# Kernel tuning notes

Hardware: AMD Instinct MI355X
Metric: run time of the kernel (lower is better)

Reference implementation:

```python
import jax, jax.numpy as jnp
import numpy as np

N_NODES = 50000
N_EDGES = 500000
D = 128
R = 8
L = 2
BN_EPS = 1e-5


def setup_inputs() -> dict:
    key = jax.random.key(0)
    ks = jax.random.split(key, 8)
    x = jax.random.normal(ks[0], (N_NODES, D), dtype=jnp.float32)
    xe = jax.random.normal(ks[1], (N_EDGES, D), dtype=jnp.float32)
    edge_index = jax.random.randint(ks[2], (2, N_EDGES), 0, N_NODES, dtype=jnp.int64)
    edge_type = jax.random.randint(ks[3], (N_EDGES,), 0, R, dtype=jnp.int64)
    # glorot init for weight/root, zeros bias; BN affine params
    w_scale = jnp.sqrt(6.0 / (D + D))
    weight = jax.random.uniform(ks[4], (L, R, D, D), jnp.float32, -w_scale, w_scale)
    root = jax.random.uniform(ks[5], (L, D, D), jnp.float32, -w_scale, w_scale)
    bias = jnp.zeros((L, D), jnp.float32)
    bn_gamma = jnp.ones((L, D), jnp.float32)
    bn_beta = jnp.zeros((L, D), jnp.float32)
    return {"x": x, "xe": xe, "edge_index": edge_index, "edge_type": edge_type,
            "weight": weight, "root": root, "bias": bias,
            "bn_gamma": bn_gamma, "bn_beta": bn_beta}


def _rgcn_edge_conv(h, xe, src, dst, etype, w, rt, b):
    # message: relu(x_j + xe) per edge (independent of relation mask)
    m = jax.nn.relu(h[src] + xe)                         # [E, D]
    # mean-aggregate per (relation, dst) via a combined segment id
    n = h.shape[0]
    seg = etype * n + dst                                # [E]
    sums = jax.ops.segment_sum(m, seg, num_segments=R * n)            # [R*N, D]
    cnt = jax.ops.segment_sum(jnp.ones((m.shape[0],), m.dtype), seg,
                              num_segments=R * n)                     # [R*N]
    mean = sums / jnp.maximum(cnt, 1.0)[:, None]
    hr = mean.reshape(R, n, -1)                          # [R, N, D]
    out = jnp.einsum('rnd,rdo->no', hr, w)               # sum_i H_i @ W_i
    out = out + h @ rt + b
    return out


def _batch_norm(h, gamma, beta):
    mu = h.mean(axis=0)
    var = jnp.mean((h - mu) ** 2, axis=0)  # biased, as torch BN (training)
    return (h - mu) * jax.lax.rsqrt(var + BN_EPS) * gamma + beta


def reference(x, xe, edge_index, edge_type, weight, root, bias, bn_gamma, bn_beta):
    src, dst = edge_index[0], edge_index[1]
    h = x
    for l in range(L):
        h = _rgcn_edge_conv(h, xe, src, dst, edge_type, weight[l], root[l], bias[l])
        h = _batch_norm(h, bn_gamma[l], bn_beta[l])
        if l != L - 1:
            h = jax.nn.relu(h)
        # drop_ratio=0 -> dropout is identity
    return h  # JK='last'
```

## Files before the change

### kernel.cpp

```cpp
#include <hip/hip_runtime.h>
#include <hip/hip_bf16.h>

typedef __attribute__((ext_vector_type(8))) short bf16x8;
typedef __attribute__((ext_vector_type(4))) float f32x4;

constexpr int D = 128;
constexpr int R = 8;
constexpr float BN_EPS = 1e-5f;

__device__ __forceinline__ unsigned short f2bf(float x) {
  __hip_bfloat16 b = __float2bfloat16(x);
  union { __hip_bfloat16 b; unsigned short u; } c; c.b = b; return c.u;
}

__global__ __launch_bounds__(256) void hist_k(const int* __restrict__ ei,
                                              const int* __restrict__ et,
                                              int* __restrict__ cnt, int E) {
  int e = blockIdx.x * 256 + threadIdx.x;
  if (e >= E) return;
  atomicAdd(&cnt[ei[E + e] * 8 + et[e]], 1);
}

__global__ __launch_bounds__(256) void scan_partial_k(const int* __restrict__ cnt,
                                                      int* __restrict__ offs,
                                                      int* __restrict__ bsum, int NK) {
  __shared__ int s[256];
  int tid = threadIdx.x;
  int base = blockIdx.x * 4096 + tid * 16;
  int loc[16];
  int sum = 0;
  #pragma unroll
  for (int i = 0; i < 16; ++i) {
    int idx = base + i;
    int v = (idx < NK) ? cnt[idx] : 0;
    loc[i] = sum; sum += v;
  }
  s[tid] = sum;
  __syncthreads();
  if (tid == 0) {
    int run = 0;
    for (int i = 0; i < 256; ++i) { int t = s[i]; s[i] = run; run += t; }
    bsum[blockIdx.x] = run;
  }
  __syncthreads();
  int off = s[tid];
  #pragma unroll
  for (int i = 0; i < 16; ++i) {
    int idx = base + i;
    if (idx < NK) offs[idx] = off + loc[i];
  }
}

__global__ void scan_bsums_k(int* __restrict__ bsum, int nb) {
  if (threadIdx.x == 0 && blockIdx.x == 0) {
    int run = 0;
    for (int b = 0; b < nb; ++b) { int t = bsum[b]; bsum[b] = run; run += t; }
  }
}

__global__ __launch_bounds__(256) void scan_addback_k(int* __restrict__ offs,
                                                      const int* __restrict__ bsum,
                                                      int NK, int E) {
  int idx = blockIdx.x * 256 + threadIdx.x;
  if (idx < NK) offs[idx] += bsum[idx >> 12];
  if (idx == 0) offs[NK] = E;
}

__global__ __launch_bounds__(256) void place_k(const int* __restrict__ ei,
                                               const int* __restrict__ et,
                                               const int* __restrict__ offs,
                                               int* __restrict__ cnt,
                                               int2* __restrict__ pairs, int E) {
  int e = blockIdx.x * 256 + threadIdx.x;
  if (e >= E) return;
  int key = ei[E + e] * 8 + et[e];
  int pos = offs[key] + atomicAdd(&cnt[key], 1);
  pairs[pos] = make_int2(e, ei[e]);
}

__device__ __forceinline__ void edge_acc(float4& acc, int e, int s, int c,
                                         const float* __restrict__ h,
                                         const float* __restrict__ xe) {
  float4 xv = ((const float4*)xe)[(size_t)e * 32 + c];
  float4 hv = ((const float4*)h)[(size_t)s * 32 + c];
  acc.x += fmaxf(xv.x + hv.x, 0.f);
  acc.y += fmaxf(xv.y + hv.y, 0.f);
  acc.z += fmaxf(xv.z + hv.z, 0.f);
  acc.w += fmaxf(xv.w + hv.w, 0.f);
}

__global__ __launch_bounds__(256) void agg_k(const float* __restrict__ h,
                                             const float* __restrict__ xe,
                                             const int2* __restrict__ pairs,
                                             const int* __restrict__ offs,
                                             unsigned short* __restrict__ Mb, int NK) {
  int grp = threadIdx.x >> 5;
  int s0 = (blockIdx.x * 8 + grp) * 4;
  if (s0 >= NK) return;
  int c = threadIdx.x & 31;

  int4 ov = *(const int4*)(offs + s0);
  int o4 = offs[s0 + 4];
  int st[4] = {ov.x, ov.y, ov.z, ov.w};
  int en[4] = {ov.y, ov.z, ov.w, o4};

  int2 pr[4];
  #pragma unroll
  for (int j = 0; j < 4; ++j) {
    int m = en[j] - st[j];
    if (m > 0) pr[j] = pairs[st[j] + min(c, min(m, 32) - 1)];
  }

  float4 acc[4];
  #pragma unroll
  for (int j = 0; j < 4; ++j) acc[j] = make_float4(0.f, 0.f, 0.f, 0.f);

  #pragma unroll
  for (int j = 0; j < 4; ++j) {
    int m = en[j] - st[j];
    if (m > 0) {
      int mm = min(m, 32);
      {
        int e0 = __shfl(pr[j].x, 0, 32), sB = __shfl(pr[j].y, 0, 32);
        edge_acc(acc[j], e0, sB, c, h, xe);
      }
      if (mm >= 2) { edge_acc(acc[j], __shfl(pr[j].x, 1, 32), __shfl(pr[j].y, 1, 32), c, h, xe); }
      if (mm >= 3) { edge_acc(acc[j], __shfl(pr[j].x, 2, 32), __shfl(pr[j].y, 2, 32), c, h, xe); }
      if (mm >= 4) { edge_acc(acc[j], __shfl(pr[j].x, 3, 32), __shfl(pr[j].y, 3, 32), c, h, xe); }
      for (int i = 4; i < mm; ++i)
        edge_acc(acc[j], __shfl(pr[j].x, i, 32), __shfl(pr[j].y, i, 32), c, h, xe);
      for (int base = st[j] + 32; base < en[j]; base += 32) {
        int mm2 = min(32, en[j] - base);
        int2 pr2 = pairs[base + min(c, mm2 - 1)];
        for (int i = 0; i < mm2; ++i)
          edge_acc(acc[j], __shfl(pr2.x, i, 32), __shfl(pr2.y, i, 32), c, h, xe);
      }
    }
  }

  int pos = (c >> 3) * 32 + (c & 3) * 8 + ((c >> 2) & 1) * 4;
  #pragma unroll
  for (int j = 0; j < 4; ++j) {
    int len = en[j] - st[j];
    float inv = (len > 0) ? 1.0f / (float)len : 0.f;
    ushort4 u;
    u.x = f2bf(acc[j].x * inv); u.y = f2bf(acc[j].y * inv);
    u.z = f2bf(acc[j].z * inv); u.w = f2bf(acc[j].w * inv);
    *(ushort4*)(Mb + (size_t)(s0 + j) * 128 + pos) = u;
  }
}

__global__ __launch_bounds__(256) void cast_swz_k(const float* __restrict__ in,
                                                  unsigned short* __restrict__ outb, int n4) {
  int gi = blockIdx.x * 256 + threadIdx.x;
  if (gi >= n4) return;
  int n = gi >> 5, c = gi & 31;
  float4 v = ((const float4*)in)[gi];
  int pos = (c >> 3) * 32 + (c & 3) * 8 + ((c >> 2) & 1) * 4;
  ushort4 u;
  u.x = f2bf(v.x); u.y = f2bf(v.y); u.z = f2bf(v.z); u.w = f2bf(v.w);
  *(ushort4*)(outb + (size_t)n * 128 + pos) = u;
}

__global__ __launch_bounds__(256) void wcast_k(const float* __restrict__ W,
                                               const float* __restrict__ root,
                                               unsigned short* __restrict__ Whi) {
  int idx = blockIdx.x * 256 + threadIdx.x;
  if (idx >= 1152 * 128) return;
  int k = idx >> 7, col = idx & 127;
  float w = (k < 1024) ? W[idx] : root[idx - 1024 * 128];
  int kk = k & 31;
  int pos = (k & ~31) + ((kk & 15) >> 2) * 8 + (kk >> 4) * 4 + (kk & 3);
  Whi[col * 1152 + pos] = f2bf(w);
}

__global__ __launch_bounds__(256) void gemm_k(
    const unsigned short* __restrict__ Mb,
    const unsigned short* __restrict__ hb,
    const unsigned short* __restrict__ Whi,
    const float* __restrict__ bias,
    float* __restrict__ out,
    float* __restrict__ colstats, int N) {
  __shared__ float ldsS[128], ldsQ[128];
  const int tid = threadIdx.x;
  const int wv = tid >> 6, lane = tid & 63;
  const int lr = lane & 15, g = lane >> 4;
  const int r0 = blockIdx.x * 128;
  const int cf0 = wv * 2;

  int row[8];
  #pragma unroll
  for (int rf = 0; rf < 8; ++rf) row[rf] = min(r0 + rf * 16 + lr, N - 1);

  const unsigned short* pb0 = Whi + (size_t)(cf0 * 16 + lr) * 1152 + g * 8;
  const unsigned short* pb1 = pb0 + 16 * 1152;

  f32x4 acc[8][2];
  #pragma unroll
  for (int a = 0; a < 8; ++a)
    #pragma unroll
    for (int b = 0; b < 2; ++b) acc[a][b] = (f32x4){0.f, 0.f, 0.f, 0.f};

  #pragma unroll 2
  for (int t = 0; t < 32; ++t) {
    bf16x8 b0 = *(const bf16x8*)(pb0 + t * 32);
    bf16x8 b1 = *(const bf16x8*)(pb1 + t * 32);
    #pragma unroll
    for (int rf = 0; rf < 8; ++rf) {
      bf16x8 a = *(const bf16x8*)(Mb + (size_t)row[rf] * 1024 + t * 32 + g * 8);
      acc[rf][0] = __builtin_amdgcn_mfma_f32_16x16x32_bf16(a, b0, acc[rf][0], 0, 0, 0);
      acc[rf][1] = __builtin_amdgcn_mfma_f32_16x16x32_bf16(a, b1, acc[rf][1], 0, 0, 0);
    }
  }
  #pragma unroll
  for (int tt = 0; tt < 4; ++tt) {
    bf16x8 b0 = *(const bf16x8*)(pb0 + 1024 + tt * 32);
    bf16x8 b1 = *(const bf16x8*)(pb1 + 1024 + tt * 32);
    #pragma unroll
    for (int rf = 0; rf < 8; ++rf) {
      bf16x8 a = *(const bf16x8*)(hb + (size_t)row[rf] * 128 + tt * 32 + g * 8);
      acc[rf][0] = __builtin_amdgcn_mfma_f32_16x16x32_bf16(a, b0, acc[rf][0], 0, 0, 0);
      acc[rf][1] = __builtin_amdgcn_mfma_f32_16x16x32_bf16(a, b1, acc[rf][1], 0, 0, 0);
    }
  }

  #pragma unroll
  for (int c = 0; c < 2; ++c) {
    int col = (cf0 + c) * 16 + lr;
    float bs = bias[col];
    float s = 0.f, q = 0.f;
    #pragma unroll
    for (int rf = 0; rf < 8; ++rf) {
      #pragma unroll
      for (int j = 0; j < 4; ++j) {
        int r = r0 + rf * 16 + g * 4 + j;
        if (r < N) {
          float v = acc[rf][c][j] + bs;
          out[(size_t)r * 128 + col] = v;
          s += v; q += v * v;
        }
      }
    }
    s += __shfl_xor(s, 16); s += __shfl_xor(s, 32);
    q += __shfl_xor(q, 16); q += __shfl_xor(q, 32);
    if (g == 0) { ldsS[col] = s; ldsQ[col] = q; }
  }
  __syncthreads();
  if (tid < 128) {
    atomicAdd(&colstats[tid], ldsS[tid]);
    atomicAdd(&colstats[128 + tid], ldsQ[tid]);
  }
}

__global__ __launch_bounds__(256) void bn_apply_k(
    const float* __restrict__ in, float* __restrict__ out,
    unsigned short* __restrict__ hbOut,
    const float* __restrict__ colstats,
    const float* __restrict__ gamma, const float* __restrict__ beta,
    int N, int doRelu) {
  int gi = blockIdx.x * 256 + threadIdx.x;
  if (gi >= N * 32) return;
  int n = gi >> 5, c = gi & 31;
  int c0 = c * 4;
  float invN = 1.0f / (float)N;
  float4 v = ((const float4*)in)[gi];
  float4 o;
  #pragma unroll
  for (int j = 0; j < 4; ++j) {
    int cc = c0 + j;
    float mu = colstats[cc] * invN;
    float var = colstats[128 + cc] * invN - mu * mu;
    float scale = rsqrtf(var + BN_EPS) * gamma[cc];
    float shift = beta[cc] - mu * scale;
    float x = (j == 0) ? v.x : (j == 1) ? v.y : (j == 2) ? v.z : v.w;
    float y = x * scale + shift;
    if (doRelu) y = fmaxf(y, 0.f);
    if (j == 0) o.x = y; else if (j == 1) o.y = y; else if (j == 2) o.z = y; else o.w = y;
  }
  ((float4*)out)[gi] = o;
  if (hbOut) {
    int pos = (c >> 3) * 32 + (c & 3) * 8 + ((c >> 2) & 1) * 4;
    ushort4 u;
    u.x = f2bf(o.x); u.y = f2bf(o.y); u.z = f2bf(o.z); u.w = f2bf(o.w);
    *(ushort4*)(hbOut + (size_t)n * 128 + pos) = u;
  }
}

extern "C" void kernel_launch(void* const* d_in, const int* in_sizes, int n_in,
                              void* d_out, int out_size, void* d_ws, size_t ws_size,
                              hipStream_t stream) {
  const float* x      = (const float*)d_in[0];
  const float* xe     = (const float*)d_in[1];
  const int*   ei     = (const int*)d_in[2];
  const int*   et     = (const int*)d_in[3];
  const float* weight = (const float*)d_in[4];
  const float* root   = (const float*)d_in[5];
  const float* bias   = (const float*)d_in[6];
  const float* gamma  = (const float*)d_in[7];
  const float* beta   = (const float*)d_in[8];
  float* out = (float*)d_out;

  const int N = in_sizes[0] / D;
  const int E = in_sizes[3];
  const int NK = N * R;

  char* w = (char*)d_ws;
  size_t off = 0;
  auto alloc = [&](size_t bytes) { char* p = w + off; off = (off + bytes + 255) & ~(size_t)255; return p; };
  unsigned short* Mb   = (unsigned short*)alloc((size_t)NK * 128 * 2);
  unsigned short* hb   = (unsigned short*)alloc((size_t)N * 128 * 2);
  float*          h1   = (float*)alloc((size_t)N * 128 * 4);
  unsigned short* Whi  = (unsigned short*)alloc(1152 * 128 * 2);
  int*            offs = (int*)alloc((size_t)(NK + 1) * 4);
  int*            cnt  = (int*)alloc((size_t)NK * 4);
  int2*           pairs= (int2*)alloc((size_t)E * 8);
  int*            bsum = (int*)alloc(512 * 4);
  float*          cst  = (float*)alloc(256 * 4);

  const int NB = (NK + 4095) / 4096;

  hipMemsetAsync(cnt, 0, (size_t)NK * 4, stream);
  hist_k<<<(E + 255) / 256, 256, 0, stream>>>(ei, et, cnt, E);
  scan_partial_k<<<NB, 256, 0, stream>>>(cnt, offs, bsum, NK);
  scan_bsums_k<<<1, 64, 0, stream>>>(bsum, NB);
  scan_addback_k<<<(NK + 255) / 256, 256, 0, stream>>>(offs, bsum, NK, E);
  hipMemsetAsync(cnt, 0, (size_t)NK * 4, stream);
  place_k<<<(E + 255) / 256, 256, 0, stream>>>(ei, et, offs, cnt, pairs, E);

  const int aggBlocks  = (NK + 31) / 32;
  const int gemmBlocks = (N + 127) / 128;
  const int castBlocks = (N * 32 + 255) / 256;

  for (int l = 0; l < 2; ++l) {
    const float* hin = (l == 0) ? x : h1;
    float* opre      = (l == 0) ? h1 : out;

    wcast_k<<<576, 256, 0, stream>>>(weight + (size_t)l * 1024 * 128,
                                     root + (size_t)l * 128 * 128, Whi);
    agg_k<<<aggBlocks, 256, 0, stream>>>(hin, xe, pairs, offs, Mb, NK);
    if (l == 0)
      cast_swz_k<<<castBlocks, 256, 0, stream>>>(x, hb, N * 32);
    hipMemsetAsync(cst, 0, 256 * 4, stream);
    gemm_k<<<gemmBlocks, 256, 0, stream>>>(Mb, hb, Whi,
                                           bias + (size_t)l * D, opre, cst, N);
    bn_apply_k<<<castBlocks, 256, 0, stream>>>(
        opre, opre, (l == 0) ? hb : (unsigned short*)nullptr,
        cst, gamma + (size_t)l * D, beta + (size_t)l * D, N, (l == 0) ? 1 : 0);
  }
}
```

Baseline: 484.3 us.

## Cache edge features as bf16 in edge-sorted order and prefetch GEMM A tiles

In layer 0 the aggregation kernel writes each edge's features, converted to bf16, into a buffer ordered by sorted edge position. Layer 1 then reads this compact buffer sequentially instead of gathering fp32 xe rows at random, which halves the bytes and makes the reads contiguous. The GEMM merges its relation and root loops into one loop and register-prefetches the next A fragments to hide load latency. The cost is an extra 128MB write in layer 0, bf16 rounding of xe in layer 1, and higher register pressure in the GEMM.

```diff
diff --git a/kernel.cpp b/kernel.cpp
--- a/kernel.cpp
+++ b/kernel.cpp
@@ -11,6 +11,9 @@
 __device__ __forceinline__ unsigned short f2bf(float x) {
   __hip_bfloat16 b = __float2bfloat16(x);
   union { __hip_bfloat16 b; unsigned short u; } c; c.b = b; return c.u;
+}
+__device__ __forceinline__ float bf2f(unsigned short u) {
+  union { float f; unsigned int i; } c; c.i = ((unsigned int)u) << 16; return c.f;
 }
 
 __global__ __launch_bounds__(256) void hist_k(const int* __restrict__ ei,
@@ -78,10 +81,21 @@
   pairs[pos] = make_int2(e, ei[e]);
 }
 
-__device__ __forceinline__ void edge_acc(float4& acc, int e, int s, int c,
-                                         const float* __restrict__ h,
-                                         const float* __restrict__ xe) {
-  float4 xv = ((const float4*)xe)[(size_t)e * 32 + c];
+template <int XMODE>
+__device__ __forceinline__ void edge_proc(float4& acc, int pos, int e, int s, int c,
+                                          const float* __restrict__ h,
+                                          const float* __restrict__ xe,
+                                          unsigned short* __restrict__ xep) {
+  float4 xv;
+  if (XMODE == 0) {
+    xv = ((const float4*)xe)[(size_t)e * 32 + c];
+    ushort4 u;
+    u.x = f2bf(xv.x); u.y = f2bf(xv.y); u.z = f2bf(xv.z); u.w = f2bf(xv.w);
+    *(ushort4*)(xep + (size_t)pos * 128 + c * 4) = u;
+  } else {
+    ushort4 u = *(const ushort4*)(xep + (size_t)pos * 128 + c * 4);
+    xv.x = bf2f(u.x); xv.y = bf2f(u.y); xv.z = bf2f(u.z); xv.w = bf2f(u.w);
+  }
   float4 hv = ((const float4*)h)[(size_t)s * 32 + c];
   acc.x += fmaxf(xv.x + hv.x, 0.f);
   acc.y += fmaxf(xv.y + hv.y, 0.f);
@@ -89,8 +103,10 @@
   acc.w += fmaxf(xv.w + hv.w, 0.f);
 }
 
+template <int XMODE>
 __global__ __launch_bounds__(256) void agg_k(const float* __restrict__ h,
                                              const float* __restrict__ xe,
+                                             unsigned short* __restrict__ xep,
                                              const int2* __restrict__ pairs,
                                              const int* __restrict__ offs,
                                              unsigned short* __restrict__ Mb, int NK) {
@@ -115,28 +131,31 @@
   #pragma unroll
   for (int j = 0; j < 4; ++j) acc[j] = make_float4(0.f, 0.f, 0.f, 0.f);
 
+#define EP(j, i) edge_proc<XMODE>(acc[j], st[j] + (i), \
+    (XMODE == 0) ? __shfl(pr[j].x, (i), 32) : 0, \
+    __shfl(pr[j].y, (i), 32), c, h, xe, xep)
+
   #pragma unroll
   for (int j = 0; j < 4; ++j) {
     int m = en[j] - st[j];
     if (m > 0) {
       int mm = min(m, 32);
-      {
-        int e0 = __shfl(pr[j].x, 0, 32), sB = __shfl(pr[j].y, 0, 32);
-        edge_acc(acc[j], e0, sB, c, h, xe);
-      }
-      if (mm >= 2) { edge_acc(acc[j], __shfl(pr[j].x, 1, 32), __shfl(pr[j].y, 1, 32), c, h, xe); }
-      if (mm >= 3) { edge_acc(acc[j], __shfl(pr[j].x, 2, 32), __shfl(pr[j].y, 2, 32), c, h, xe); }
-      if (mm >= 4) { edge_acc(acc[j], __shfl(pr[j].x, 3, 32), __shfl(pr[j].y, 3, 32), c, h, xe); }
-      for (int i = 4; i < mm; ++i)
-        edge_acc(acc[j], __shfl(pr[j].x, i, 32), __shfl(pr[j].y, i, 32), c, h, xe);
+      EP(j, 0);
+      if (mm >= 2) EP(j, 1);
+      if (mm >= 3) EP(j, 2);
+      if (mm >= 4) EP(j, 3);
+      for (int i = 4; i < mm; ++i) EP(j, i);
       for (int base = st[j] + 32; base < en[j]; base += 32) {
         int mm2 = min(32, en[j] - base);
         int2 pr2 = pairs[base + min(c, mm2 - 1)];
         for (int i = 0; i < mm2; ++i)
-          edge_acc(acc[j], __shfl(pr2.x, i, 32), __shfl(pr2.y, i, 32), c, h, xe);
+          edge_proc<XMODE>(acc[j], base + i,
+                           (XMODE == 0) ? __shfl(pr2.x, i, 32) : 0,
+                           __shfl(pr2.y, i, 32), c, h, xe, xep);
       }
     }
   }
+#undef EP
 
   int pos = (c >> 3) * 32 + (c & 3) * 8 + ((c >> 2) & 1) * 4;
   #pragma unroll
@@ -201,27 +220,32 @@
     #pragma unroll
     for (int b = 0; b < 2; ++b) acc[a][b] = (f32x4){0.f, 0.f, 0.f, 0.f};
 
+  auto aload = [&](int t, int rf) -> bf16x8 {
+    if (t < 32)
+      return *(const bf16x8*)(Mb + (size_t)row[rf] * 1024 + t * 32 + g * 8);
+    return *(const bf16x8*)(hb + (size_t)row[rf] * 128 + (t - 32) * 32 + g * 8);
+  };
+
+  bf16x8 a_cur[8];
+  #pragma unroll
+  for (int rf = 0; rf < 8; ++rf) a_cur[rf] = aload(0, rf);
+
   #pragma unroll 2
-  for (int t = 0; t < 32; ++t) {
+  for (int t = 0; t < 36; ++t) {
+    bf16x8 a_nxt[8];
+    if (t < 35) {
+      #pragma unroll
+      for (int rf = 0; rf < 8; ++rf) a_nxt[rf] = aload(t + 1, rf);
+    }
     bf16x8 b0 = *(const bf16x8*)(pb0 + t * 32);
     bf16x8 b1 = *(const bf16x8*)(pb1 + t * 32);
     #pragma unroll
     for (int rf = 0; rf < 8; ++rf) {
-      bf16x8 a = *(const bf16x8*)(Mb + (size_t)row[rf] * 1024 + t * 32 + g * 8);
-      acc[rf][0] = __builtin_amdgcn_mfma_f32_16x16x32_bf16(a, b0, acc[rf][0], 0, 0, 0);
-      acc[rf][1] = __builtin_amdgcn_mfma_f32_16x16x32_bf16(a, b1, acc[rf][1], 0, 0, 0);
+      acc[rf][0] = __builtin_amdgcn_mfma_f32_16x16x32_bf16(a_cur[rf], b0, acc[rf][0], 0, 0, 0);
+      acc[rf][1] = __builtin_amdgcn_mfma_f32_16x16x32_bf16(a_cur[rf], b1, acc[rf][1], 0, 0, 0);
     }
-  }
-  #pragma unroll
-  for (int tt = 0; tt < 4; ++tt) {
-    bf16x8 b0 = *(const bf16x8*)(pb0 + 1024 + tt * 32);
-    bf16x8 b1 = *(const bf16x8*)(pb1 + 1024 + tt * 32);
     #pragma unroll
-    for (int rf = 0; rf < 8; ++rf) {
-      bf16x8 a = *(const bf16x8*)(hb + (size_t)row[rf] * 128 + tt * 32 + g * 8);
-      acc[rf][0] = __builtin_amdgcn_mfma_f32_16x16x32_bf16(a, b0, acc[rf][0], 0, 0, 0);
-      acc[rf][1] = __builtin_amdgcn_mfma_f32_16x16x32_bf16(a, b1, acc[rf][1], 0, 0, 0);
-    }
+    for (int rf = 0; rf < 8; ++rf) a_cur[rf] = a_nxt[rf];
   }
 
   #pragma unroll
@@ -308,6 +332,7 @@
   size_t off = 0;
   auto alloc = [&](size_t bytes) { char* p = w + off; off = (off + bytes + 255) & ~(size_t)255; return p; };
   unsigned short* Mb   = (unsigned short*)alloc((size_t)NK * 128 * 2);
+  unsigned short* xep  = (unsigned short*)alloc((size_t)E * 128 * 2);
   unsigned short* hb   = (unsigned short*)alloc((size_t)N * 128 * 2);
   float*          h1   = (float*)alloc((size_t)N * 128 * 4);
   unsigned short* Whi  = (unsigned short*)alloc(1152 * 128 * 2);
@@ -337,7 +362,10 @@
 
     wcast_k<<<576, 256, 0, stream>>>(weight + (size_t)l * 1024 * 128,
                                      root + (size_t)l * 128 * 128, Whi);
-    agg_k<<<aggBlocks, 256, 0, stream>>>(hin, xe, pairs, offs, Mb, NK);
+    if (l == 0)
+      agg_k<0><<<aggBlocks, 256, 0, stream>>>(hin, xe, xep, pairs, offs, Mb, NK);
+    else
+      agg_k<1><<<aggBlocks, 256, 0, stream>>>(hin, xe, xep, pairs, offs, Mb, NK);
     if (l == 0)
       cast_swz_k<<<castBlocks, 256, 0, stream>>>(x, hb, N * 32);
     hipMemsetAsync(cst, 0, 256 * 4, stream);
```

New measurement: 496.3 us. 1.02x slower.

## Fold layer-1 batchnorm and ReLU into layer-2 gather and cast

Applied to the files above, without the earlier changes.

Drops the separate BN-apply pass after layer 1. A tiny kernel now turns the column stats into per-column scale and shift, and the layer-2 aggregation and cast kernels apply the affine transform plus ReLU on the fly as they read h1. The layer-2 aggregation also walks segments in reverse order, apparently to hit data the previous kernels left in L2. The trade is extra FMAs on every gathered edge row (500K edges times 128 columns) instead of one elementwise pass over N×128, which saves a full read and write of h1.

```diff
diff --git a/kernel.cpp b/kernel.cpp
--- a/kernel.cpp
+++ b/kernel.cpp
@@ -78,26 +78,59 @@
   pairs[pos] = make_int2(e, ei[e]);
 }
 
+__global__ void bnprep_k(const float* __restrict__ colstats,
+                         const float* __restrict__ gamma,
+                         const float* __restrict__ beta,
+                         float* __restrict__ sc, float* __restrict__ sh, int N) {
+  int c = threadIdx.x;
+  float invN = 1.0f / (float)N;
+  float mu = colstats[c] * invN;
+  float var = colstats[128 + c] * invN - mu * mu;
+  float scale = rsqrtf(var + BN_EPS) * gamma[c];
+  sc[c] = scale;
+  sh[c] = beta[c] - mu * scale;
+}
+
+template <int AFF>
 __device__ __forceinline__ void edge_acc(float4& acc, int e, int s, int c,
                                          const float* __restrict__ h,
-                                         const float* __restrict__ xe) {
+                                         const float* __restrict__ xe,
+                                         const float4 scv, const float4 shv) {
   float4 xv = ((const float4*)xe)[(size_t)e * 32 + c];
   float4 hv = ((const float4*)h)[(size_t)s * 32 + c];
+  if (AFF) {
+    hv.x = fmaxf(fmaf(hv.x, scv.x, shv.x), 0.f);
+    hv.y = fmaxf(fmaf(hv.y, scv.y, shv.y), 0.f);
+    hv.z = fmaxf(fmaf(hv.z, scv.z, shv.z), 0.f);
+    hv.w = fmaxf(fmaf(hv.w, scv.w, shv.w), 0.f);
+  }
   acc.x += fmaxf(xv.x + hv.x, 0.f);
   acc.y += fmaxf(xv.y + hv.y, 0.f);
   acc.z += fmaxf(xv.z + hv.z, 0.f);
   acc.w += fmaxf(xv.w + hv.w, 0.f);
 }
 
+template <int AFF>
 __global__ __launch_bounds__(256) void agg_k(const float* __restrict__ h,
                                              const float* __restrict__ xe,
                                              const int2* __restrict__ pairs,
                                              const int* __restrict__ offs,
-                                             unsigned short* __restrict__ Mb, int NK) {
+                                             const float* __restrict__ sc,
+                                             const float* __restrict__ sh,
+                                             unsigned short* __restrict__ Mb,
+                                             int NK, int rev) {
   int grp = threadIdx.x >> 5;
-  int s0 = (blockIdx.x * 8 + grp) * 4;
-  if (s0 >= NK) return;
+  int idx = blockIdx.x * 8 + grp;
+  if (idx * 4 >= NK) return;
+  if (rev) idx = (NK >> 2) - 1 - idx;
+  int s0 = idx * 4;
   int c = threadIdx.x & 31;
+
+  float4 scv = make_float4(0.f, 0.f, 0.f, 0.f), shv = scv;
+  if (AFF) {
+    scv = *(const float4*)(sc + c * 4);
+    shv = *(const float4*)(sh + c * 4);
+  }
 
   int4 ov = *(const int4*)(offs + s0);
   int o4 = offs[s0 + 4];
@@ -115,28 +148,29 @@
   #pragma unroll
   for (int j = 0; j < 4; ++j) acc[j] = make_float4(0.f, 0.f, 0.f, 0.f);
 
+#define EP(j, i) edge_acc<AFF>(acc[j], __shfl(pr[j].x, (i), 32), \
+                               __shfl(pr[j].y, (i), 32), c, h, xe, scv, shv)
+
   #pragma unroll
   for (int j = 0; j < 4; ++j) {
     int m = en[j] - st[j];
     if (m > 0) {
       int mm = min(m, 32);
-      {
-        int e0 = __shfl(pr[j].x, 0, 32), sB = __shfl(pr[j].y, 0, 32);
-        edge_acc(acc[j], e0, sB, c, h, xe);
-      }
-      if (mm >= 2) { edge_acc(acc[j], __shfl(pr[j].x, 1, 32), __shfl(pr[j].y, 1, 32), c, h, xe); }
-      if (mm >= 3) { edge_acc(acc[j], __shfl(pr[j].x, 2, 32), __shfl(pr[j].y, 2, 32), c, h, xe); }
-      if (mm >= 4) { edge_acc(acc[j], __shfl(pr[j].x, 3, 32), __shfl(pr[j].y, 3, 32), c, h, xe); }
-      for (int i = 4; i < mm; ++i)
-        edge_acc(acc[j], __shfl(pr[j].x, i, 32), __shfl(pr[j].y, i, 32), c, h, xe);
+      EP(j, 0);
+      if (mm >= 2) EP(j, 1);
+      if (mm >= 3) EP(j, 2);
+      if (mm >= 4) EP(j, 3);
+      for (int i = 4; i < mm; ++i) EP(j, i);
       for (int base = st[j] + 32; base < en[j]; base += 32) {
         int mm2 = min(32, en[j] - base);
         int2 pr2 = pairs[base + min(c, mm2 - 1)];
         for (int i = 0; i < mm2; ++i)
-          edge_acc(acc[j], __shfl(pr2.x, i, 32), __shfl(pr2.y, i, 32), c, h, xe);
+          edge_acc<AFF>(acc[j], __shfl(pr2.x, i, 32), __shfl(pr2.y, i, 32),
+                        c, h, xe, scv, shv);
       }
     }
   }
+#undef EP
 
   int pos = (c >> 3) * 32 + (c & 3) * 8 + ((c >> 2) & 1) * 4;
   #pragma unroll
@@ -150,12 +184,24 @@
   }
 }
 
+template <int AFF>
 __global__ __launch_bounds__(256) void cast_swz_k(const float* __restrict__ in,
-                                                  unsigned short* __restrict__ outb, int n4) {
+                                                  unsigned short* __restrict__ outb,
+                                                  const float* __restrict__ sc,
+                                                  const float* __restrict__ sh,
+                                                  int n4) {
   int gi = blockIdx.x * 256 + threadIdx.x;
   if (gi >= n4) return;
   int n = gi >> 5, c = gi & 31;
   float4 v = ((const float4*)in)[gi];
+  if (AFF) {
+    float4 scv = *(const float4*)(sc + c * 4);
+    float4 shv = *(const float4*)(sh + c * 4);
+    v.x = fmaxf(fmaf(v.x, scv.x, shv.x), 0.f);
+    v.y = fmaxf(fmaf(v.y, scv.y, shv.y), 0.f);
+    v.z = fmaxf(fmaf(v.z, scv.z, shv.z), 0.f);
+    v.w = fmaxf(fmaf(v.w, scv.w, shv.w), 0.f);
+  }
   int pos = (c >> 3) * 32 + (c & 3) * 8 + ((c >> 2) & 1) * 4;
   ushort4 u;
   u.x = f2bf(v.x); u.y = f2bf(v.y); u.z = f2bf(v.z); u.w = f2bf(v.w);
@@ -254,14 +300,11 @@
 
 __global__ __launch_bounds__(256) void bn_apply_k(
     const float* __restrict__ in, float* __restrict__ out,
-    unsigned short* __restrict__ hbOut,
     const float* __restrict__ colstats,
-    const float* __restrict__ gamma, const float* __restrict__ beta,
-    int N, int doRelu) {
+    const float* __restrict__ gamma, const float* __restrict__ beta, int N) {
   int gi = blockIdx.x * 256 + threadIdx.x;
   if (gi >= N * 32) return;
-  int n = gi >> 5, c = gi & 31;
-  int c0 = c * 4;
+  int c0 = (gi & 31) * 4;
   float invN = 1.0f / (float)N;
   float4 v = ((const float4*)in)[gi];
   float4 o;
@@ -274,16 +317,9 @@
     float shift = beta[cc] - mu * scale;
     float x = (j == 0) ? v.x : (j == 1) ? v.y : (j == 2) ? v.z : v.w;
     float y = x * scale + shift;
-    if (doRelu) y = fmaxf(y, 0.f);
     if (j == 0) o.x = y; else if (j == 1) o.y = y; else if (j == 2) o.z = y; else o.w = y;
   }
   ((float4*)out)[gi] = o;
-  if (hbOut) {
-    int pos = (c >> 3) * 32 + (c & 3) * 8 + ((c >> 2) & 1) * 4;
-    ushort4 u;
-    u.x = f2bf(o.x); u.y = f2bf(o.y); u.z = f2bf(o.z); u.w = f2bf(o.w);
-    *(ushort4*)(hbOut + (size_t)n * 128 + pos) = u;
-  }
 }
 
 extern "C" void kernel_launch(void* const* d_in, const int* in_sizes, int n_in,
@@ -315,7 +351,10 @@
   int*            cnt  = (int*)alloc((size_t)NK * 4);
   int2*           pairs= (int2*)alloc((size_t)E * 8);
   int*            bsum = (int*)alloc(512 * 4);
-  float*          cst  = (float*)alloc(256 * 4);
+  float*          cst0 = (float*)alloc(256 * 4);
+  float*          cst1 = (float*)alloc(256 * 4);
+  float*          sc   = (float*)alloc(128 * 4);
+  float*          sh   = (float*)alloc(128 * 4);
 
   const int NB = (NK + 4095) / 4096;
 
@@ -331,20 +370,20 @@
   const int gemmBlocks = (N + 127) / 128;
   const int castBlocks = (N * 32 + 255) / 256;
 
-  for (int l = 0; l < 2; ++l) {
-    const float* hin = (l == 0) ? x : h1;
-    float* opre      = (l == 0) ? h1 : out;
-
-    wcast_k<<<576, 256, 0, stream>>>(weight + (size_t)l * 1024 * 128,
-                                     root + (size_t)l * 128 * 128, Whi);
-    agg_k<<<aggBlocks, 256, 0, stream>>>(hin, xe, pairs, offs, Mb, NK);
-    if (l == 0)
-      cast_swz_k<<<castBlocks, 256, 0, stream>>>(x, hb, N * 32);
-    hipMemsetAsync(cst, 0, 256 * 4, stream);
-    gemm_k<<<gemmBlocks, 256, 0, stream>>>(Mb, hb, Whi,
-                                           bias + (size_t)l * D, opre, cst, N);
-    bn_apply_k<<<castBlocks, 256, 0, stream>>>(
-        opre, opre, (l == 0) ? hb : (unsigned short*)nullptr,
-        cst, gamma + (size_t)l * D, beta + (size_t)l * D, N, (l == 0) ? 1 : 0);
-  }
-}
+  wcast_k<<<576, 256, 0, stream>>>(weight, root, Whi);
+  agg_k<0><<<aggBlocks, 256, 0, stream>>>(x, xe, pairs, offs, nullptr, nullptr,
+                                          Mb, NK, 0);
+  cast_swz_k<0><<<castBlocks, 256, 0, stream>>>(x, hb, nullptr, nullptr, N * 32);
+  hipMemsetAsync(cst0, 0, 256 * 4, stream);
+  gemm_k<<<gemmBlocks, 256, 0, stream>>>(Mb, hb, Whi, bias, h1, cst0, N);
+  bnprep_k<<<1, 128, 0, stream>>>(cst0, gamma, beta, sc, sh, N);
+
+  wcast_k<<<576, 256, 0, stream>>>(weight + (size_t)1024 * 128,
+                                   root + (size_t)128 * 128, Whi);
+  agg_k<1><<<aggBlocks, 256, 0, stream>>>(h1, xe, pairs, offs, sc, sh,
+                                          Mb, NK, 1 );
+  cast_swz_k<1><<<castBlocks, 256, 0, stream>>>(h1, hb, sc, sh, N * 32);
+  hipMemsetAsync(cst1, 0, 256 * 4, stream);
+  gemm_k<<<gemmBlocks, 256, 0, stream>>>(Mb, hb, Whi, bias + D, out, cst1, N);
+  bn_apply_k<<<castBlocks, 256, 0, stream>>>(out, out, cst1, gamma + D, beta + D, N);
+}
```

Result: no change. 477.2 us (-1.5%).
